# Kernel optimization log

Hardware: AMD Instinct MI355X
Metric: run time of the kernel (lower is better)

The kernel has to match this reference:

```python
import jax, jax.numpy as jnp
import numpy as np

EMBED_DIM = 1024
NUM_HEADS = 16
HEAD_DIM = EMBED_DIM // NUM_HEADS
SCALE = HEAD_DIM ** -0.5
B, S = 4, 2048


def setup_inputs() -> dict:
    key = jax.random.key(0)
    ks = jax.random.split(key, 11)
    std = EMBED_DIM ** -0.5
    return {
        "query": jax.random.normal(ks[0], (B, S, EMBED_DIM), jnp.float32),
        "key": jax.random.normal(ks[1], (B, S, EMBED_DIM), jnp.float32),
        "value": jax.random.normal(ks[2], (B, S, EMBED_DIM), jnp.float32),
        "Wq": jax.random.normal(ks[3], (EMBED_DIM, EMBED_DIM), jnp.float32) * std,
        "bq": jax.random.normal(ks[4], (EMBED_DIM,), jnp.float32) * 0.01,
        "Wk": jax.random.normal(ks[5], (EMBED_DIM, EMBED_DIM), jnp.float32) * std,
        "bk": jax.random.normal(ks[6], (EMBED_DIM,), jnp.float32) * 0.01,
        "Wv": jax.random.normal(ks[7], (EMBED_DIM, EMBED_DIM), jnp.float32) * std,
        "bv": jax.random.normal(ks[8], (EMBED_DIM,), jnp.float32) * 0.01,
        "Wo": jax.random.normal(ks[9], (EMBED_DIM, EMBED_DIM), jnp.float32) * std,
        "bo": jax.random.normal(ks[10], (EMBED_DIM,), jnp.float32) * 0.01,
    }


def reference(query, key, value, Wq, bq, Wk, bk, Wv, bv, Wo, bo):
    b, s, _ = query.shape
    # torch.nn.Linear: x @ W.T + b
    q = query @ Wq.T + bq
    k = key @ Wk.T + bk
    v = value @ Wv.T + bv
    # [b, h, s, d]
    q = q.reshape(b, s, NUM_HEADS, HEAD_DIM).transpose(0, 2, 1, 3)
    k = k.reshape(b, s, NUM_HEADS, HEAD_DIM).transpose(0, 2, 1, 3)
    v = v.reshape(b, s, NUM_HEADS, HEAD_DIM).transpose(0, 2, 1, 3)
    # explicit scores [b, h, s, s]
    scores = jnp.einsum("bhqd,bhkd->bhqk", q, k) * SCALE
    causal = jnp.tril(jnp.ones((s, s), dtype=bool))  # is_causal=True
    scores = jnp.where(causal, scores, -jnp.inf)
    attn = jax.nn.softmax(scores, axis=-1)
    out = jnp.einsum("bhqk,bhkd->bhqd", attn, v)
    out = out.transpose(0, 2, 1, 3).reshape(b, s, EMBED_DIM)
    return out @ Wo.T + bo
```

## Files before the change

### kernel.cpp

```cpp
#include <hip/hip_runtime.h>


#define E 1024
#define HEADS 16
#define HD 64
#define SEQ 2048
#define BATCH 4
#define MROWS (BATCH * SEQ)

typedef __bf16 bf16x8 __attribute__((ext_vector_type(8)));
typedef __bf16 bf16x2 __attribute__((ext_vector_type(2)));
typedef float f32x4 __attribute__((ext_vector_type(4)));
typedef unsigned short ushort8v __attribute__((ext_vector_type(8)));

typedef __attribute__((address_space(1))) void gvoid;
typedef __attribute__((address_space(3))) void lvoid;

__device__ __forceinline__ void async16(const void* g, void* l) {
  __builtin_amdgcn_global_load_lds((gvoid*)g, (lvoid*)l, 16, 0, 0);
}

__device__ __forceinline__ unsigned short f2bf(float f) {
  union { float f; unsigned int u; } v;
  v.f = f;
  unsigned int r = v.u + 0x7FFFu + ((v.u >> 16) & 1u);
  return (unsigned short)(r >> 16);
}

__device__ __forceinline__ unsigned packbf(float a, float b) {
  bf16x2 t;
  t[0] = (__bf16)a;
  t[1] = (__bf16)b;
  return __builtin_bit_cast(unsigned, t);
}

__device__ __forceinline__ void store_out(unsigned short* p, float v) { *p = f2bf(v); }
__device__ __forceinline__ void store_out(float* p, float v) { *p = v; }

struct CastArgs {
  const float* src[4];
  unsigned short* dst[4];
  int n;
};

__global__ __launch_bounds__(256) void cast_kernel(CastArgs a) {
  const float* s = a.src[blockIdx.z];
  unsigned short* d = a.dst[blockIdx.z];
  const int n = a.n;
  const int stride = gridDim.x * blockDim.x * 4;
  for (int i = (blockIdx.x * blockDim.x + threadIdx.x) * 4; i < n; i += stride) {
    float4 v = *(const float4*)(s + i);
    ushort4 o;
    o.x = f2bf(v.x); o.y = f2bf(v.y); o.z = f2bf(v.z); o.w = f2bf(v.w);
    *(ushort4*)(d + i) = o;
  }
}

template <typename OutT>
__device__ __forceinline__ void gemm_body(const unsigned short* __restrict__ A,
                                          const unsigned short* __restrict__ W,
                                          const float* __restrict__ bias,
                                          OutT* __restrict__ out, float scale) {
  __shared__ unsigned short At[128 * 64];
  __shared__ unsigned short Wt[128 * 64];
  const int tid = threadIdx.x;
  const int lane = tid & 63;
  const int wv = tid >> 6;
  const int wm = wv & 1, wn = wv >> 1;
  const int li = lane & 15, g = lane >> 4;
  const int m0 = blockIdx.x * 128, n0 = blockIdx.y * 128;
  f32x4 acc[4][4] = {};

  for (int k0 = 0; k0 < E; k0 += 64) {
    __syncthreads();
#pragma unroll
    for (int i = 0; i < 4; ++i) {
      int c = tid + 256 * i;
      int row = c >> 3, slot = c & 7;
      int gc = slot ^ (row & 7);
      async16(A + (size_t)(m0 + row) * E + k0 + gc * 8, &At[c * 8]);
      async16(W + (size_t)(n0 + row) * E + k0 + gc * 8, &Wt[c * 8]);
    }
    asm volatile("s_waitcnt vmcnt(0)" ::: "memory");
    __syncthreads();
#pragma unroll
    for (int kk = 0; kk < 2; ++kk) {
      bf16x8 af[4], bfr[4];
#pragma unroll
      for (int mt = 0; mt < 4; ++mt) {
        int r = wm * 64 + mt * 16 + li;
        int slot = (kk * 4 + g) ^ (r & 7);
        af[mt] = *(const bf16x8*)&At[r * 64 + slot * 8];
      }
#pragma unroll
      for (int nt = 0; nt < 4; ++nt) {
        int r = wn * 64 + nt * 16 + li;
        int slot = (kk * 4 + g) ^ (r & 7);
        bfr[nt] = *(const bf16x8*)&Wt[r * 64 + slot * 8];
      }
#pragma unroll
      for (int mt = 0; mt < 4; ++mt)
#pragma unroll
        for (int nt = 0; nt < 4; ++nt)
          acc[mt][nt] =
              __builtin_amdgcn_mfma_f32_16x16x32_bf16(af[mt], bfr[nt], acc[mt][nt], 0, 0, 0);
    }
  }

#pragma unroll
  for (int nt = 0; nt < 4; ++nt) {
    int col = n0 + wn * 64 + nt * 16 + li;
    float bv = bias[col];
#pragma unroll
    for (int mt = 0; mt < 4; ++mt) {
#pragma unroll
      for (int r = 0; r < 4; ++r) {
        int row = m0 + wm * 64 + mt * 16 + g * 4 + r;
        store_out(&out[(size_t)row * E + col], (acc[mt][nt][r] + bv) * scale);
      }
    }
  }
}

struct QkvArgs {
  const unsigned short* A[3];
  const unsigned short* W[3];
  const float* bias[3];
  unsigned short* out[3];
  float scale[3];
};

__global__ __launch_bounds__(256) void gemm_qkv(QkvArgs p) {
  const int z = blockIdx.z;
  gemm_body<unsigned short>(p.A[z], p.W[z], p.bias[z], p.out[z], p.scale[z]);
}

__global__ __launch_bounds__(256) void gemm_out_k(const unsigned short* __restrict__ A,
                                                  const unsigned short* __restrict__ W,
                                                  const float* __restrict__ bias,
                                                  float* __restrict__ out) {
  gemm_body<float>(A, W, bias, out, 1.0f);
}

__global__ __launch_bounds__(256, 2) void flash_kernel(const unsigned short* __restrict__ Qb,
                                                       const unsigned short* __restrict__ Kb,
                                                       const unsigned short* __restrict__ Vb,
                                                       unsigned short* __restrict__ Ob) {
  __shared__ unsigned short Kt[2][128 * 64];
  __shared__ unsigned short Vt[2][64 * 128];
  const int p = blockIdx.x;
  const int bh = blockIdx.y;
  const int b = bh >> 4, h16 = bh & 15;
  const size_t base = (size_t)b * SEQ * E + (size_t)h16 * HD;
  const unsigned short* Qp = Qb + base;
  const unsigned short* Kp = Kb + base;
  const unsigned short* Vp = Vb + base;
  unsigned short* Op = Ob + base;
  const int tid = threadIdx.x, lane = tid & 63, wv = tid >> 6;
  const int li = lane & 15, g = lane >> 4;
  const int qlo = p, qhi = 15 - p;
  const int slo = ((g & 1) << 5) | li;

  bf16x8 qfL[2][2], qfH[2][2];
#pragma unroll
  for (int mt = 0; mt < 2; ++mt)
#pragma unroll
    for (int kk = 0; kk < 2; ++kk) {
      int rl = qlo * 128 + wv * 32 + mt * 16 + li;
      int rh = qhi * 128 + wv * 32 + mt * 16 + li;
      qfL[mt][kk] = *(const bf16x8*)(Qp + (size_t)rl * E + kk * 32 + g * 8);
      qfH[mt][kk] = *(const bf16x8*)(Qp + (size_t)rh * E + kk * 32 + g * 8);
    }

  f32x4 oaL[4][2] = {}, oaH[4][2] = {};
  float miL[2] = {-1e30f, -1e30f}, lsL[2] = {0.0f, 0.0f};
  float miH[2] = {-1e30f, -1e30f}, lsH[2] = {0.0f, 0.0f};

  ushort8v vv[4];

  auto loadV = [&](int j) {
#pragma unroll
    for (int i = 0; i < 4; ++i) {
      int c = tid + 256 * i;
      int key = c & 127, db = (c >> 7) * 8;
      vv[i] = *(const ushort8v*)(Vp + (size_t)(j * 128 + key) * E + db);
    }
  };
  auto stageK = [&](int j, int buf) {
#pragma unroll
    for (int i = 0; i < 4; ++i) {
      int c = tid + 256 * i;
      int row = c >> 3, slot = c & 7;
      int gc = slot ^ (row & 7);
      async16(Kp + (size_t)(j * 128 + row) * E + gc * 8, &Kt[buf][c * 8]);
    }
  };
  auto scatV = [&](int buf) {
#pragma unroll
    for (int i = 0; i < 4; ++i) {
      int c = tid + 256 * i;
      int key = c & 127, db = (c >> 7) * 8;
#pragma unroll
      for (int jj = 0; jj < 8; ++jj) {
        int n = db + jj;
        int slot = (key >> 3) ^ (n & 15);
        Vt[buf][n * 128 + slot * 8 + (key & 7)] = vv[i][jj];
      }
    }
  };

  auto compute = [&](const bf16x8 (&qf)[2][2], float (&mi)[2], float (&ls)[2],
                     f32x4 (&oa)[4][2], bool diag, int buf) {
#pragma unroll
    for (int h = 0; h < 2; ++h) {
      if (diag && h * 64 > wv * 32 + 31) continue;

      f32x4 sacc[4][2] = {};
#pragma unroll
      for (int kk = 0; kk < 2; ++kk) {
        bf16x8 kf[4];
#pragma unroll
        for (int nt = 0; nt < 4; ++nt) {
          int key = h * 64 + nt * 16 + li;
          int slot = (kk * 4 + g) ^ (key & 7);
          kf[nt] = *(const bf16x8*)&Kt[buf][key * 64 + slot * 8];
        }
#pragma unroll
        for (int nt = 0; nt < 4; ++nt)
#pragma unroll
          for (int mt = 0; mt < 2; ++mt)
            sacc[nt][mt] =
                __builtin_amdgcn_mfma_f32_16x16x32_bf16(kf[nt], qf[mt][kk], sacc[nt][mt], 0, 0, 0);
      }

      if (diag && h * 64 + 63 > wv * 32) {
#pragma unroll
        for (int nt = 0; nt < 4; ++nt)
#pragma unroll
          for (int mt = 0; mt < 2; ++mt)
#pragma unroll
            for (int r = 0; r < 4; ++r) {
              int keyg = h * 64 + nt * 16 + g * 4 + r;
              int qg = wv * 32 + mt * 16 + li;
              sacc[nt][mt][r] = (keyg > qg) ? -1e30f : sacc[nt][mt][r];
            }
      }

      float alpha[2];
#pragma unroll
      for (int mt = 0; mt < 2; ++mt) {
        float mx = sacc[0][mt][0];
#pragma unroll
        for (int nt = 0; nt < 4; ++nt)
#pragma unroll
          for (int r = 0; r < 4; ++r) mx = fmaxf(mx, sacc[nt][mt][r]);
        mx = fmaxf(mx, __shfl_xor(mx, 16));
        mx = fmaxf(mx, __shfl_xor(mx, 32));
        float mnew = fmaxf(mi[mt], mx);
        alpha[mt] = __expf(mi[mt] - mnew);
        mi[mt] = mnew;
      }

      unsigned pk[4][2][2];
      float rs[2] = {0.0f, 0.0f};
#pragma unroll
      for (int nt = 0; nt < 4; ++nt)
#pragma unroll
        for (int mt = 0; mt < 2; ++mt) {
          float p0 = __expf(sacc[nt][mt][0] - mi[mt]);
          float p1 = __expf(sacc[nt][mt][1] - mi[mt]);
          float p2 = __expf(sacc[nt][mt][2] - mi[mt]);
          float p3 = __expf(sacc[nt][mt][3] - mi[mt]);
          rs[mt] += (p0 + p1) + (p2 + p3);
          pk[nt][mt][0] = packbf(p0, p1);
          pk[nt][mt][1] = packbf(p2, p3);
        }
#pragma unroll
      for (int mt = 0; mt < 2; ++mt) {
        float s = rs[mt];
        s += __shfl_xor(s, 16);
        s += __shfl_xor(s, 32);
        ls[mt] = ls[mt] * alpha[mt] + s;
#pragma unroll
        for (int dt = 0; dt < 4; ++dt) oa[dt][mt] *= alpha[mt];
      }

#pragma unroll
      for (int kk2 = 0; kk2 < 2; ++kk2) {
        const int kc = h * 2 + kk2;
        bf16x8 vf[4];
#pragma unroll
        for (int dt = 0; dt < 4; ++dt) {
          int d = dt * 16 + li;
          int slot = (kc * 4 + g) ^ (d & 15);
          vf[dt] = *(const bf16x8*)&Vt[buf][d * 128 + slot * 8];
        }
#pragma unroll
        for (int mt = 0; mt < 2; ++mt) {
          int a0 = __shfl((int)pk[kk2 * 2][mt][0], slo);
          int a1 = __shfl((int)pk[kk2 * 2][mt][1], slo);
          int a2 = __shfl((int)pk[kk2 * 2][mt][0], slo + 16);
          int a3 = __shfl((int)pk[kk2 * 2][mt][1], slo + 16);
          int c0 = __shfl((int)pk[kk2 * 2 + 1][mt][0], slo);
          int c1 = __shfl((int)pk[kk2 * 2 + 1][mt][1], slo);
          int c2 = __shfl((int)pk[kk2 * 2 + 1][mt][0], slo + 16);
          int c3 = __shfl((int)pk[kk2 * 2 + 1][mt][1], slo + 16);
          bool hi = (g & 2) != 0;
          uint4 bb;
          bb.x = hi ? c0 : a0;
          bb.y = hi ? c1 : a1;
          bb.z = hi ? c2 : a2;
          bb.w = hi ? c3 : a3;
          bf16x8 pf = __builtin_bit_cast(bf16x8, bb);
#pragma unroll
          for (int dt = 0; dt < 4; ++dt)
            oa[dt][mt] =
                __builtin_amdgcn_mfma_f32_16x16x32_bf16(vf[dt], pf, oa[dt][mt], 0, 0, 0);
        }
      }
    }
  };

  loadV(0);
  stageK(0, 0);
  scatV(0);

  for (int j = 0; j <= qhi; ++j) {
    const int buf = j & 1;
    asm volatile("s_waitcnt vmcnt(0)" ::: "memory");
    __syncthreads();
    if (j < qhi) {
      loadV(j + 1);
      stageK(j + 1, buf ^ 1);
    }
    compute(qfH, miH, lsH, oaH, j == qhi, buf);
    if (j <= qlo) compute(qfL, miL, lsL, oaL, j == qlo, buf);
    if (j < qhi) scatV(buf ^ 1);
  }

#pragma unroll
  for (int t = 0; t < 2; ++t) {
    const int qt = t ? qhi : qlo;
    f32x4(&oa)[4][2] = t ? oaH : oaL;
    float* ls = t ? lsH : lsL;
#pragma unroll
    for (int mt = 0; mt < 2; ++mt) {
      float inv = 1.0f / ls[mt];
      int row = qt * 128 + wv * 32 + mt * 16 + li;
#pragma unroll
      for (int dt = 0; dt < 4; ++dt) {
        ushort4 w;
        w.x = f2bf(oa[dt][mt][0] * inv);
        w.y = f2bf(oa[dt][mt][1] * inv);
        w.z = f2bf(oa[dt][mt][2] * inv);
        w.w = f2bf(oa[dt][mt][3] * inv);
        *(ushort4*)(Op + (size_t)row * E + dt * 16 + g * 4) = w;
      }
    }
  }
}

extern "C" void kernel_launch(void* const* d_in, const int* in_sizes, int n_in,
                              void* d_out, int out_size, void* d_ws, size_t ws_size,
                              hipStream_t stream) {
  const float* q  = (const float*)d_in[0];
  const float* k  = (const float*)d_in[1];
  const float* v  = (const float*)d_in[2];
  const float* Wq = (const float*)d_in[3];
  const float* bq = (const float*)d_in[4];
  const float* Wk = (const float*)d_in[5];
  const float* bk = (const float*)d_in[6];
  const float* Wv = (const float*)d_in[7];
  const float* bv = (const float*)d_in[8];
  const float* Wo = (const float*)d_in[9];
  const float* bo = (const float*)d_in[10];

  unsigned short* Xq  = (unsigned short*)d_ws;
  unsigned short* Xk  = Xq + (size_t)MROWS * E;
  unsigned short* Xv  = Xk + (size_t)MROWS * E;
  unsigned short* Wqb = Xv + (size_t)MROWS * E;
  unsigned short* Wkb = Wqb + (size_t)E * E;
  unsigned short* Wvb = Wkb + (size_t)E * E;
  unsigned short* Wob = Wvb + (size_t)E * E;
  unsigned short* Qb  = Wob + (size_t)E * E;
  unsigned short* Kb  = Qb + (size_t)MROWS * E;
  unsigned short* Vb  = Kb + (size_t)MROWS * E;
  unsigned short* Og  = Xq;

  CastArgs ca;
  ca.src[0] = q; ca.src[1] = k; ca.src[2] = v; ca.src[3] = nullptr;
  ca.dst[0] = Xq; ca.dst[1] = Xk; ca.dst[2] = Xv; ca.dst[3] = nullptr;
  ca.n = MROWS * E;
  cast_kernel<<<dim3(1024, 1, 3), 256, 0, stream>>>(ca);

  CastArgs cw;
  cw.src[0] = Wq; cw.src[1] = Wk; cw.src[2] = Wv; cw.src[3] = Wo;
  cw.dst[0] = Wqb; cw.dst[1] = Wkb; cw.dst[2] = Wvb; cw.dst[3] = Wob;
  cw.n = E * E;
  cast_kernel<<<dim3(256, 1, 4), 256, 0, stream>>>(cw);

  QkvArgs p;
  p.A[0] = Xq;  p.A[1] = Xk;  p.A[2] = Xv;
  p.W[0] = Wqb; p.W[1] = Wkb; p.W[2] = Wvb;
  p.bias[0] = bq; p.bias[1] = bk; p.bias[2] = bv;
  p.out[0] = Qb; p.out[1] = Kb; p.out[2] = Vb;
  p.scale[0] = 0.125f; p.scale[1] = 1.0f; p.scale[2] = 1.0f;
  gemm_qkv<<<dim3(64, 8, 3), 256, 0, stream>>>(p);

  flash_kernel<<<dim3(8, 64), 256, 0, stream>>>(Qb, Kb, Vb, Og);

  gemm_out_k<<<dim3(64, 8), 256, 0, stream>>>(Og, Wob, bo, (float*)d_out);
}
```

Baseline: 405.7 us.

## Single-buffer V tile in flash kernel for occupancy; merge cast launches

The flash attention kernel drops double buffering of the transposed V tile in shared memory, freeing LDS so three blocks per CU can be resident (launch bounds raised to 3). The V scatter now happens at the top of each iteration behind an extra barrier, so the register-held V prefetch is no longer overlapped with compute. Separately, the activation and weight fp32-to-bf16 casts are merged into one launch over seven tensors with per-tensor lengths, removing one kernel launch. The risk is more barrier stalls and less load/compute overlap in exchange for higher occupancy and possible register pressure under the tighter bound.

Measured after the change: 555.1 us. +36.8%, slower.

```diff
diff --git a/kernel.cpp b/kernel.cpp
--- a/kernel.cpp
+++ b/kernel.cpp
@@ -38,15 +38,15 @@
 __device__ __forceinline__ void store_out(float* p, float v) { *p = v; }
 
 struct CastArgs {
-  const float* src[4];
-  unsigned short* dst[4];
-  int n;
+  const float* src[7];
+  unsigned short* dst[7];
+  int n[7];
 };
 
 __global__ __launch_bounds__(256) void cast_kernel(CastArgs a) {
   const float* s = a.src[blockIdx.z];
   unsigned short* d = a.dst[blockIdx.z];
-  const int n = a.n;
+  const int n = a.n[blockIdx.z];
   const int stride = gridDim.x * blockDim.x * 4;
   for (int i = (blockIdx.x * blockDim.x + threadIdx.x) * 4; i < n; i += stride) {
     float4 v = *(const float4*)(s + i);
@@ -142,12 +142,12 @@
   gemm_body<float>(A, W, bias, out, 1.0f);
 }
 
-__global__ __launch_bounds__(256, 2) void flash_kernel(const unsigned short* __restrict__ Qb,
+__global__ __launch_bounds__(256, 3) void flash_kernel(const unsigned short* __restrict__ Qb,
                                                        const unsigned short* __restrict__ Kb,
                                                        const unsigned short* __restrict__ Vb,
                                                        unsigned short* __restrict__ Ob) {
   __shared__ unsigned short Kt[2][128 * 64];
-  __shared__ unsigned short Vt[2][64 * 128];
+  __shared__ unsigned short Vt[64 * 128];
   const int p = blockIdx.x;
   const int bh = blockIdx.y;
   const int b = bh >> 4, h16 = bh & 15;
@@ -195,7 +195,7 @@
       async16(Kp + (size_t)(j * 128 + row) * E + gc * 8, &Kt[buf][c * 8]);
     }
   };
-  auto scatV = [&](int buf) {
+  auto scatV = [&]() {
 #pragma unroll
     for (int i = 0; i < 4; ++i) {
       int c = tid + 256 * i;
@@ -204,7 +204,7 @@
       for (int jj = 0; jj < 8; ++jj) {
         int n = db + jj;
         int slot = (key >> 3) ^ (n & 15);
-        Vt[buf][n * 128 + slot * 8 + (key & 7)] = vv[i][jj];
+        Vt[n * 128 + slot * 8 + (key & 7)] = vv[i][jj];
       }
     }
   };
@@ -293,7 +293,7 @@
         for (int dt = 0; dt < 4; ++dt) {
           int d = dt * 16 + li;
           int slot = (kc * 4 + g) ^ (d & 15);
-          vf[dt] = *(const bf16x8*)&Vt[buf][d * 128 + slot * 8];
+          vf[dt] = *(const bf16x8*)&Vt[d * 128 + slot * 8];
         }
 #pragma unroll
         for (int mt = 0; mt < 2; ++mt) {
@@ -323,19 +323,19 @@
 
   loadV(0);
   stageK(0, 0);
-  scatV(0);
 
   for (int j = 0; j <= qhi; ++j) {
     const int buf = j & 1;
     asm volatile("s_waitcnt vmcnt(0)" ::: "memory");
     __syncthreads();
+    scatV();
+    __syncthreads();
     if (j < qhi) {
       loadV(j + 1);
       stageK(j + 1, buf ^ 1);
     }
     compute(qfH, miH, lsH, oaH, j == qhi, buf);
     if (j <= qlo) compute(qfL, miL, lsL, oaL, j == qlo, buf);
-    if (j < qhi) scatV(buf ^ 1);
   }
 
 #pragma unroll
@@ -388,16 +388,14 @@
   unsigned short* Og  = Xq;
 
   CastArgs ca;
-  ca.src[0] = q; ca.src[1] = k; ca.src[2] = v; ca.src[3] = nullptr;
-  ca.dst[0] = Xq; ca.dst[1] = Xk; ca.dst[2] = Xv; ca.dst[3] = nullptr;
-  ca.n = MROWS * E;
-  cast_kernel<<<dim3(1024, 1, 3), 256, 0, stream>>>(ca);
-
-  CastArgs cw;
-  cw.src[0] = Wq; cw.src[1] = Wk; cw.src[2] = Wv; cw.src[3] = Wo;
-  cw.dst[0] = Wqb; cw.dst[1] = Wkb; cw.dst[2] = Wvb; cw.dst[3] = Wob;
-  cw.n = E * E;
-  cast_kernel<<<dim3(256, 1, 4), 256, 0, stream>>>(cw);
+  ca.src[0] = q;  ca.dst[0] = Xq;  ca.n[0] = MROWS * E;
+  ca.src[1] = k;  ca.dst[1] = Xk;  ca.n[1] = MROWS * E;
+  ca.src[2] = v;  ca.dst[2] = Xv;  ca.n[2] = MROWS * E;
+  ca.src[3] = Wq; ca.dst[3] = Wqb; ca.n[3] = E * E;
+  ca.src[4] = Wk; ca.dst[4] = Wkb; ca.n[4] = E * E;
+  ca.src[5] = Wv; ca.dst[5] = Wvb; ca.n[5] = E * E;
+  ca.src[6] = Wo; ca.dst[6] = Wob; ca.n[6] = E * E;
+  cast_kernel<<<dim3(512, 1, 7), 256, 0, stream>>>(ca);
 
   QkvArgs p;
   p.A[0] = Xq;  p.A[1] = Xk;  p.A[2] = Xv;
```
